# Kernel tuning notes

Hardware: AMD Instinct MI355X
Metric: run time of the kernel (lower is better)

The kernel has to match this reference:

```python
import jax, jax.numpy as jnp
import numpy as np

B, S, D, H, L, FF = 32, 512, 256, 8, 2, 512
E = 64  # embed_dim_per_feature
VOCABS = [20, 50, 100]
NCLS = 36
MAX_CONN, THR = 10, 0.6


def _ln(x, g, b, eps=1e-5):
    m = x.mean(-1, keepdims=True)
    v = ((x - m) ** 2).mean(-1, keepdims=True)
    return g * (x - m) / jnp.sqrt(v + eps) + b


def _build_adj(cat, cnt):
    # self loops + chain links + banded similarity links (create_mutation_graph_optimized)
    Bb, _, Ss = cat.shape
    adj = jnp.broadcast_to(jnp.eye(Ss, dtype=jnp.float32), (Bb, Ss, Ss))
    for d in range(1, MAX_CONN):
        if d >= Ss:
            break
        cat_sim = (cat[:, :, :-d] == cat[:, :, d:]).astype(jnp.float32).mean(1)
        cnt_sim = jnp.exp(-jnp.abs(cnt[:, :-d] - cnt[:, d:]) / 100.0)
        sim = 0.5 * (cat_sim + cnt_sim)  # [B, S-d]
        base = 1.0 if d == 1 else 0.0  # chain link stays 1 when sim<=thr
        val = jnp.where(sim > THR, sim, base)
        ii = jnp.arange(Ss - d)
        adj = adj.at[:, ii, ii + d].set(val)
        adj = adj.at[:, ii + d, ii].set(val)
    return adj


def setup_inputs():
    key = jax.random.key(0)
    ks = iter(jax.random.split(key, 40))
    def nrm(shape, s=0.02):
        return jax.random.normal(next(ks), shape, jnp.float32) * s
    return {
        "categorical_x": jax.random.randint(next(ks), (B, 3, S), 0, min(VOCABS)),
        "count_x": jax.random.uniform(next(ks), (B, S), jnp.float32) * 100.0,
        "emb0": nrm((VOCABS[0], E)), "emb1": nrm((VOCABS[1], E)), "emb2": nrm((VOCABS[2], E)),
        "cnt_W": nrm((1, E)), "cnt_b": jnp.zeros((E,), jnp.float32),
        "pos_enc": nrm((S, D)),
        "gat_W": nrm((L, D, D)), "gat_a": nrm((L, 2 * D, 1)),
        "qkv_W": nrm((L, 3 * D, D)), "qkv_b": jnp.zeros((L, 3 * D), jnp.float32),
        "outp_W": nrm((L, D, D)), "outp_b": jnp.zeros((L, D), jnp.float32),
        "ff1_W": nrm((L, FF, D)), "ff1_b": jnp.zeros((L, FF), jnp.float32),
        "ff2_W": nrm((L, D, FF)), "ff2_b": jnp.zeros((L, D), jnp.float32),
        "ln_g": jnp.ones((L, 3, D), jnp.float32), "ln_b": jnp.zeros((L, 3, D), jnp.float32),
        "cls1_W": nrm((D // 2, D)), "cls1_b": jnp.zeros((D // 2,), jnp.float32),
        "cls2_W": nrm((NCLS, D // 2)), "cls2_b": jnp.zeros((NCLS,), jnp.float32),
    }


def reference(categorical_x, count_x, emb0, emb1, emb2, cnt_W, cnt_b, pos_enc,
              gat_W, gat_a, qkv_W, qkv_b, outp_W, outp_b,
              ff1_W, ff1_b, ff2_W, ff2_b, ln_g, ln_b,
              cls1_W, cls1_b, cls2_W, cls2_b):
    Ss = categorical_x.shape[2]
    # per-timestep feature embedding + count projection, concat -> d_model
    x = jnp.concatenate([
        emb0[categorical_x[:, 0]], emb1[categorical_x[:, 1]], emb2[categorical_x[:, 2]],
        count_x[..., None] @ cnt_W + cnt_b], -1)
    x = x + pos_enc[:Ss]
    mask = _build_adj(categorical_x, count_x) > 0  # adj used only as mask
    dh = D // H
    for l in range(L):
        # GraphAttentionLayer: e_ij = Wh_i.a1 + Wh_j.a2 (same math as repeat+concat+matmul)
        Wh = x @ gat_W[l]
        e = (Wh @ gat_a[l][:D, 0])[:, :, None] + (Wh @ gat_a[l][D:, 0])[:, None, :]
        att = jax.nn.softmax(jnp.where(mask, e, -9e15), -1)
        g = jax.nn.elu(att @ Wh)
        x = _ln(x + g, ln_g[l, 0], ln_b[l, 0])
        # MultiheadAttention (batch_first, eval)
        qkv = x @ qkv_W[l].T + qkv_b[l]
        q, k, v = jnp.split(qkv, 3, -1)
        q = q.reshape(-1, Ss, H, dh)
        k = k.reshape(-1, Ss, H, dh)
        v = v.reshape(-1, Ss, H, dh)
        sc = jnp.einsum('bihd,bjhd->bhij', q, k) / jnp.sqrt(jnp.float32(dh))
        o = jnp.einsum('bhij,bjhd->bihd', jax.nn.softmax(sc, -1), v).reshape(-1, Ss, D)
        o = o @ outp_W[l].T + outp_b[l]
        x = _ln(x + o, ln_g[l, 1], ln_b[l, 1])
        # FFN
        ff = jax.nn.relu(x @ ff1_W[l].T + ff1_b[l]) @ ff2_W[l].T + ff2_b[l]
        x = _ln(x + ff, ln_g[l, 2], ln_b[l, 2])
    pooled = x.mean(1)
    h = jax.nn.relu(pooled @ cls1_W.T + cls1_b)
    return h @ cls2_W.T + cls2_b
```

## Files before the change

kernel.cpp:

```cpp
#include <hip/hip_runtime.h>
#include <hip/hip_bf16.h>
#include <math.h>

#define Bn 32
#define Sn 512
#define Dn 256
#define Hn 8
#define DHn 32
#define En 64
#define FFn 512
#define Ln 2
#define NCLSn 36
#define BANDR 9
#define NBn 19
#define Mn (Bn * Sn)

typedef __attribute__((ext_vector_type(8))) short s8v;
typedef __attribute__((ext_vector_type(4))) float f4v;
typedef __attribute__((ext_vector_type(4))) unsigned short us4;
typedef unsigned short ushortT;

__device__ __forceinline__ ushortT f2b(float f) {
    unsigned u = __float_as_uint(f);
    unsigned r = (u + 0x7FFFu + ((u >> 16) & 1u)) >> 16;
    return (ushortT)r;
}

#define GLDS16(g, l)                                                            \
    __builtin_amdgcn_global_load_lds(                                           \
        (const __attribute__((address_space(1))) void*)(g),                     \
        (__attribute__((address_space(3))) void*)(l), 16, 0, 0)

__global__ void k_f2b(const float* __restrict__ in, ushortT* __restrict__ out, int n) {
    int i = (blockIdx.x * blockDim.x + threadIdx.x) * 4;
    if (i >= n) return;
    float4 v = *(const float4*)(in + i);
    out[i + 0] = f2b(v.x); out[i + 1] = f2b(v.y);
    out[i + 2] = f2b(v.z); out[i + 3] = f2b(v.w);
}

__global__ void k_f2bT(const float* __restrict__ in, ushortT* __restrict__ out) {
    int i = blockIdx.x * 256 + threadIdx.x;
    int l = i >> 16, rem = i & 65535;
    int k = rem >> 8, n = rem & 255;
    out[(l << 16) + n * 256 + k] = f2b(in[i]);
}

__global__ void k_embed(const int* __restrict__ cat, const float* __restrict__ cnt,
                        const float* __restrict__ e0, const float* __restrict__ e1,
                        const float* __restrict__ e2,
                        const float* __restrict__ cW, const float* __restrict__ cb,
                        const float* __restrict__ pos, float* __restrict__ x,
                        ushortT* __restrict__ xb) {
    int bs = blockIdx.x;
    int d = threadIdx.x;
    int b = bs >> 9, s = bs & 511;
    float v;
    if (d < 64)       v = e0[cat[(b * 3 + 0) * Sn + s] * En + d];
    else if (d < 128) v = e1[cat[(b * 3 + 1) * Sn + s] * En + (d - 64)];
    else if (d < 192) v = e2[cat[(b * 3 + 2) * Sn + s] * En + (d - 128)];
    else              v = cnt[b * Sn + s] * cW[d - 192] + cb[d - 192];
    float y = v + pos[s * Dn + d];
    x[(size_t)bs * Dn + d] = y;
    xb[(size_t)bs * Dn + d] = f2b(y);
}

__global__ void k_mask(const int* __restrict__ cat, const float* __restrict__ cnt,
                       unsigned char* __restrict__ mask) {
    int idx = blockIdx.x * blockDim.x + threadIdx.x;
    if (idx >= Bn * Sn * NBn) return;
    int off = idx % NBn;
    int bs = idx / NBn;
    int b = bs >> 9, i = bs & 511;
    int j = i + off - BANDR;
    unsigned char m = 0;
    if (j >= 0 && j < Sn) {
        int dd = off - BANDR;
        int ad = dd < 0 ? -dd : dd;
        if (ad <= 1) {
            m = 1;
        } else {
            int c = 0;
            for (int f = 0; f < 3; f++)
                c += (cat[(b * 3 + f) * Sn + i] == cat[(b * 3 + f) * Sn + j]);
            float cat_sim = (float)c / 3.0f;
            float cnt_sim = expf(-fabsf(cnt[b * Sn + i] - cnt[b * Sn + j]) / 100.0f);
            float sim = 0.5f * (cat_sim + cnt_sim);
            m = (sim > 0.6f) ? 1 : 0;
        }
    }
    mask[idx] = m;
}

template <int ACT>
__global__ __launch_bounds__(256) void k_gemm_mfma(const ushortT* __restrict__ A,
                                                   const ushortT* __restrict__ Bt,
                                                   const float* __restrict__ bias,
                                                   ushortT* __restrict__ Cout,
                                                   int M, int N, int K) {
    __shared__ ushortT As[2][128 * 32];
    __shared__ ushortT Bs[2][128 * 32];
    int tid = threadIdx.x;
    int w = tid >> 6, lane = tid & 63;
    int g = lane >> 4, lr = lane & 15;
    int m0 = blockIdx.y * 128, n0 = blockIdx.x * 128;
    int wr = w >> 1, wc = w & 1;
    int NT = K >> 5;
    f4v acc[4][4];
#pragma unroll
    for (int m = 0; m < 4; m++)
#pragma unroll
        for (int n = 0; n < 4; n++) acc[m][n] = (f4v){0.f, 0.f, 0.f, 0.f};

    auto stage = [&](int t, int buf) {
        int k0 = t << 5;
#pragma unroll
        for (int r = 0; r < 2; r++) {
            int e = (tid + r * 256) * 8;
            int row = e >> 5, kk = e & 31;
            GLDS16(A + (size_t)(m0 + row) * K + k0 + kk, &As[buf][e]);
            GLDS16(Bt + (size_t)(n0 + row) * K + k0 + kk, &Bs[buf][e]);
        }
    };

    stage(0, 0);
    __syncthreads();
    for (int t = 0; t < NT; t++) {
        int cur = t & 1;
        if (t + 1 < NT) stage(t + 1, cur ^ 1);
        s8v af[4], bf[4];
#pragma unroll
        for (int m = 0; m < 4; m++)
            af[m] = *(const s8v*)(&As[cur][(wr * 64 + m * 16 + lr) * 32 + g * 8]);
#pragma unroll
        for (int n = 0; n < 4; n++)
            bf[n] = *(const s8v*)(&Bs[cur][(wc * 64 + n * 16 + lr) * 32 + g * 8]);
#pragma unroll
        for (int m = 0; m < 4; m++)
#pragma unroll
            for (int n = 0; n < 4; n++)
                acc[m][n] = __builtin_amdgcn_mfma_f32_16x16x32_bf16(af[m], bf[n], acc[m][n], 0, 0, 0);
        __syncthreads();
    }
#pragma unroll
    for (int m = 0; m < 4; m++) {
#pragma unroll
        for (int n = 0; n < 4; n++) {
            int col = n0 + wc * 64 + n * 16 + lr;
            float bv = bias ? bias[col] : 0.0f;
#pragma unroll
            for (int r = 0; r < 4; r++) {
                int row = m0 + wr * 64 + m * 16 + g * 4 + r;
                float v = acc[m][n][r] + bv;
                if (ACT == 1) v = fmaxf(v, 0.0f);
                Cout[(size_t)row * N + col] = f2b(v);
            }
        }
    }
}

template <int MODE>
__global__ __launch_bounds__(512) void k_gemm_row(const ushortT* __restrict__ A,
                                                  const ushortT* __restrict__ Bt,
                                                  const float* __restrict__ bias,
                                                  const float* __restrict__ ga,
                                                  float* __restrict__ a1h, float* __restrict__ a2h,
                                                  float* __restrict__ Whout,
                                                  const float* __restrict__ lg,
                                                  const float* __restrict__ lb,
                                                  float* __restrict__ x, ushortT* __restrict__ xb,
                                                  int K) {
    __shared__ ushortT As[2][64 * 32];
    __shared__ ushortT Bs[2][256 * 32];
    __shared__ float red1[64][4], red2[64][4];
    int tid = threadIdx.x;
    int w = tid >> 6, lane = tid & 63;
    int g = lane >> 4, lr = lane & 15;
    int wr = w >> 2, wc = w & 3;
    int m0 = blockIdx.x * 64;
    int NT = K >> 5;
    f4v acc[2][4];
#pragma unroll
    for (int m = 0; m < 2; m++)
#pragma unroll
        for (int n = 0; n < 4; n++) acc[m][n] = (f4v){0.f, 0.f, 0.f, 0.f};

    auto stage = [&](int t, int buf) {
        int k0 = t << 5;
        if (tid < 256) {
            int e = tid * 8;
            int row = e >> 5, kk = e & 31;
            GLDS16(A + (size_t)(m0 + row) * K + k0 + kk, &As[buf][e]);
        }
#pragma unroll
        for (int r = 0; r < 2; r++) {
            int e = (tid + r * 512) * 8;
            int row = e >> 5, kk = e & 31;
            GLDS16(Bt + (size_t)row * K + k0 + kk, &Bs[buf][e]);
        }
    };

    stage(0, 0);
    __syncthreads();
    for (int t = 0; t < NT; t++) {
        int cur = t & 1;
        if (t + 1 < NT) stage(t + 1, cur ^ 1);
        s8v af[2], bf[4];
#pragma unroll
        for (int m = 0; m < 2; m++)
            af[m] = *(const s8v*)(&As[cur][(wr * 32 + m * 16 + lr) * 32 + g * 8]);
#pragma unroll
        for (int n = 0; n < 4; n++)
            bf[n] = *(const s8v*)(&Bs[cur][(wc * 64 + n * 16 + lr) * 32 + g * 8]);
#pragma unroll
        for (int m = 0; m < 2; m++)
#pragma unroll
            for (int n = 0; n < 4; n++)
                acc[m][n] = __builtin_amdgcn_mfma_f32_16x16x32_bf16(af[m], bf[n], acc[m][n], 0, 0, 0);
        __syncthreads();
    }

    int cn[4];
#pragma unroll
    for (int n = 0; n < 4; n++) cn[n] = wc * 64 + n * 16 + lr;

    if constexpr (MODE == 0) {
        float a1v[4], a2v[4];
#pragma unroll
        for (int n = 0; n < 4; n++) { a1v[n] = ga[cn[n]]; a2v[n] = ga[Dn + cn[n]]; }
#pragma unroll
        for (int m = 0; m < 2; m++)
#pragma unroll
            for (int r = 0; r < 4; r++) {
                int rowl = wr * 32 + m * 16 + g * 4 + r;
                float p1 = 0.f, p2 = 0.f;
#pragma unroll
                for (int n = 0; n < 4; n++) {
                    float v = acc[m][n][r];
                    Whout[(size_t)(m0 + rowl) * Dn + cn[n]] = v;
                    p1 += v * a1v[n];
                    p2 += v * a2v[n];
                }
                p1 += __shfl_xor(p1, 1); p2 += __shfl_xor(p2, 1);
                p1 += __shfl_xor(p1, 2); p2 += __shfl_xor(p2, 2);
                p1 += __shfl_xor(p1, 4); p2 += __shfl_xor(p2, 4);
                p1 += __shfl_xor(p1, 8); p2 += __shfl_xor(p2, 8);
                if (lr == 0) { red1[rowl][wc] = p1; red2[rowl][wc] = p2; }
            }
        __syncthreads();
        if (tid < 64) {
            float t1 = red1[tid][0] + red1[tid][1] + red1[tid][2] + red1[tid][3];
            float t2 = red2[tid][0] + red2[tid][1] + red2[tid][2] + red2[tid][3];
            a1h[m0 + tid] = t1;
            a2h[m0 + tid] = t2;
        }
    } else {
        float bv[4], lgv[4], lbv[4];
#pragma unroll
        for (int n = 0; n < 4; n++) { bv[n] = bias[cn[n]]; lgv[n] = lg[cn[n]]; lbv[n] = lb[cn[n]]; }
#pragma unroll
        for (int m = 0; m < 2; m++)
#pragma unroll
            for (int r = 0; r < 4; r++) {
                int rowl = wr * 32 + m * 16 + g * 4 + r;
                float s1 = 0.f, s2 = 0.f;
#pragma unroll
                for (int n = 0; n < 4; n++) {
                    float y = acc[m][n][r] + bv[n] + x[(size_t)(m0 + rowl) * Dn + cn[n]];
                    acc[m][n][r] = y;
                    s1 += y;
                    s2 += y * y;
                }
                s1 += __shfl_xor(s1, 1); s2 += __shfl_xor(s2, 1);
                s1 += __shfl_xor(s1, 2); s2 += __shfl_xor(s2, 2);
                s1 += __shfl_xor(s1, 4); s2 += __shfl_xor(s2, 4);
                s1 += __shfl_xor(s1, 8); s2 += __shfl_xor(s2, 8);
                if (lr == 0) { red1[rowl][wc] = s1; red2[rowl][wc] = s2; }
            }
        __syncthreads();
#pragma unroll
        for (int m = 0; m < 2; m++)
#pragma unroll
            for (int r = 0; r < 4; r++) {
                int rowl = wr * 32 + m * 16 + g * 4 + r;
                float S1 = red1[rowl][0] + red1[rowl][1] + red1[rowl][2] + red1[rowl][3];
                float S2 = red2[rowl][0] + red2[rowl][1] + red2[rowl][2] + red2[rowl][3];
                float mean = S1 * (1.0f / Dn);
                float var = S2 * (1.0f / Dn) - mean * mean;
                float rs = rsqrtf(var + 1e-5f);
#pragma unroll
                for (int n = 0; n < 4; n++) {
                    float o = lgv[n] * (acc[m][n][r] - mean) * rs + lbv[n];
                    size_t idx = (size_t)(m0 + rowl) * Dn + cn[n];
                    x[idx] = o;
                    xb[idx] = f2b(o);
                }
            }
    }
}

__global__ __launch_bounds__(256) void k_gat_attn_ln(const float* __restrict__ Wh,
                                                     const float* __restrict__ a1h,
                                                     const float* __restrict__ a2h,
                                                     const unsigned char* __restrict__ mask,
                                                     const float* __restrict__ lg,
                                                     const float* __restrict__ lb,
                                                     float* __restrict__ x,
                                                     ushortT* __restrict__ xb) {
    int w = threadIdx.x >> 6, l = threadIdx.x & 63;
    int bs = blockIdx.x * 4 + w;
    int b = bs >> 9, i = bs & 511;
    float e = -1e30f;
    int j = i + l - BANDR;
    if (l < NBn && j >= 0 && j < Sn && mask[bs * NBn + l])
        e = a1h[bs] + a2h[(b << 9) + j];
    float mx = e;
#pragma unroll
    for (int o = 32; o; o >>= 1) mx = fmaxf(mx, __shfl_xor(mx, o));
    float p = (e > -1e29f) ? __expf(e - mx) : 0.0f;
    float sum = p;
#pragma unroll
    for (int o = 32; o; o >>= 1) sum += __shfl_xor(sum, o);
    p *= (1.0f / sum);
    int c4 = l * 4;
    const float* whb = Wh + (size_t)(b << 9) * Dn + c4;
    float gx = 0.f, gy = 0.f, gz = 0.f, gw = 0.f;
#pragma unroll
    for (int o = 0; o < NBn; o++) {
        float wo = __shfl(p, o);
        int jo = i + o - BANDR;
        jo = jo < 0 ? 0 : (jo > Sn - 1 ? Sn - 1 : jo);
        float4 v = *(const float4*)(whb + (size_t)jo * Dn);
        gx += wo * v.x; gy += wo * v.y; gz += wo * v.z; gw += wo * v.w;
    }
    gx = gx > 0.f ? gx : expm1f(gx);
    gy = gy > 0.f ? gy : expm1f(gy);
    gz = gz > 0.f ? gz : expm1f(gz);
    gw = gw > 0.f ? gw : expm1f(gw);
    float4 xv = *(const float4*)(x + (size_t)bs * Dn + c4);
    float y0 = xv.x + gx, y1 = xv.y + gy, y2 = xv.z + gz, y3 = xv.w + gw;
    float s1 = y0 + y1 + y2 + y3;
    float s2 = y0 * y0 + y1 * y1 + y2 * y2 + y3 * y3;
#pragma unroll
    for (int o = 32; o; o >>= 1) {
        s1 += __shfl_xor(s1, o);
        s2 += __shfl_xor(s2, o);
    }
    float mean = s1 * (1.0f / Dn);
    float var = s2 * (1.0f / Dn) - mean * mean;
    float r = rsqrtf(var + 1e-5f);
    float4 lgv = *(const float4*)(lg + c4);
    float4 lbv = *(const float4*)(lb + c4);
    float o0 = lgv.x * (y0 - mean) * r + lbv.x;
    float o1 = lgv.y * (y1 - mean) * r + lbv.y;
    float o2 = lgv.z * (y2 - mean) * r + lbv.z;
    float o3 = lgv.w * (y3 - mean) * r + lbv.w;
    *(float4*)(x + (size_t)bs * Dn + c4) = make_float4(o0, o1, o2, o3);
    us4 ob = {f2b(o0), f2b(o1), f2b(o2), f2b(o3)};
    *(us4*)(xb + (size_t)bs * Dn + c4) = ob;
}

__global__ __launch_bounds__(256) void k_attn_mfma(const ushortT* __restrict__ qkv,
                                                   ushortT* __restrict__ ob) {
    __shared__ ushortT Ks[2][64 * 32];
    __shared__ ushortT Vt[2][32 * 64];
    __shared__ ushortT Ps[4][16 * 72];
    int tid = threadIdx.x;
    int w = tid >> 6, lane = tid & 63;
    int g = lane >> 4, lr = lane & 15;
    int blk = blockIdx.x;
    int qh = blk & 1, h = (blk >> 1) & 7, b = blk >> 4;
    const ushortT* base = qkv + (size_t)b * Sn * 768;
    const ushortT* kbase = base + 256 + h * 32;
    const ushortT* vbase = base + 512 + h * 32;

    int krow2 = tid >> 3;
    int kc = (tid & 7) ^ (krow2 & 7);
    int kkv = krow2 * 2 + (kc >> 2);
    int kdd = (kc & 3) * 8;
    int vd0 = w * 8;

    int q0 = qh * 256 + w * 64;
    s8v qf[4];
#pragma unroll
    for (int m = 0; m < 4; m++)
        qf[m] = *(const s8v*)(base + (size_t)(q0 + m * 16 + lr) * 768 + h * 32 + g * 8);

    f4v o[4][2];
    float rl[4][4];
#pragma unroll
    for (int m = 0; m < 4; m++) {
        o[m][0] = (f4v){0.f, 0.f, 0.f, 0.f};
        o[m][1] = (f4v){0.f, 0.f, 0.f, 0.f};
#pragma unroll
        for (int r = 0; r < 4; r++) rl[m][r] = 0.f;
    }
    const float scale = 0.17677669529663687f;

    {
        GLDS16(kbase + (size_t)kkv * 768 + kdd, &Ks[0][tid * 8]);
        us4 v0 = *(const us4*)(vbase + (size_t)lane * 768 + vd0);
        us4 v1 = *(const us4*)(vbase + (size_t)lane * 768 + vd0 + 4);
#pragma unroll
        for (int jj = 0; jj < 4; jj++) {
            int d = vd0 + jj;
            Vt[0][d * 64 + (lane ^ ((d & 7) << 3))] = v0[jj];
            int d2 = d + 4;
            Vt[0][d2 * 64 + (lane ^ ((d2 & 7) << 3))] = v1[jj];
        }
    }
    __syncthreads();

    for (int kt = 0; kt < 8; kt++) {
        int cur = kt & 1, nxt = cur ^ 1;
        us4 v0, v1;
        if (kt < 7) {
            GLDS16(kbase + (size_t)((kt + 1) * 64 + kkv) * 768 + kdd, &Ks[nxt][tid * 8]);
            v0 = *(const us4*)(vbase + (size_t)((kt + 1) * 64 + lane) * 768 + vd0);
            v1 = *(const us4*)(vbase + (size_t)((kt + 1) * 64 + lane) * 768 + vd0 + 4);
        }
        s8v kf[4];
#pragma unroll
        for (int n = 0; n < 4; n++) {
            int row2 = n * 8 + (lr >> 1);
            int cc = (((lr & 1) << 2) + g) ^ (row2 & 7);
            kf[n] = *(const s8v*)(&Ks[cur][row2 * 64 + cc * 8]);
        }
        s8v vf[2][2];
#pragma unroll
        for (int cd = 0; cd < 2; cd++)
#pragma unroll
            for (int c2 = 0; c2 < 2; c2++) {
                int d = cd * 16 + lr;
                vf[cd][c2] = *(const s8v*)(&Vt[cur][d * 64 + ((c2 * 32 + g * 8) ^ ((d & 7) << 3))]);
            }
#pragma unroll
        for (int m = 0; m < 4; m++) {
            f4v s[4];
#pragma unroll
            for (int n = 0; n < 4; n++) {
                f4v z = (f4v){0.f, 0.f, 0.f, 0.f};
                s[n] = __builtin_amdgcn_mfma_f32_16x16x32_bf16(qf[m], kf[n], z, 0, 0, 0);
            }
#pragma unroll
            for (int r = 0; r < 4; r++) {
                float p0 = __expf(fminf(s[0][r] * scale, 60.f));
                float p1 = __expf(fminf(s[1][r] * scale, 60.f));
                float p2 = __expf(fminf(s[2][r] * scale, 60.f));
                float p3 = __expf(fminf(s[3][r] * scale, 60.f));
                rl[m][r] += (p0 + p1) + (p2 + p3);
                int rr = g * 4 + r;
                Ps[w][rr * 72 + lr]      = f2b(p0);
                Ps[w][rr * 72 + 16 + lr] = f2b(p1);
                Ps[w][rr * 72 + 32 + lr] = f2b(p2);
                Ps[w][rr * 72 + 48 + lr] = f2b(p3);
            }
            s8v pf0 = *(const s8v*)(&Ps[w][lr * 72 + g * 8]);
            s8v pf1 = *(const s8v*)(&Ps[w][lr * 72 + 32 + g * 8]);
            o[m][0] = __builtin_amdgcn_mfma_f32_16x16x32_bf16(pf0, vf[0][0], o[m][0], 0, 0, 0);
            o[m][0] = __builtin_amdgcn_mfma_f32_16x16x32_bf16(pf1, vf[0][1], o[m][0], 0, 0, 0);
            o[m][1] = __builtin_amdgcn_mfma_f32_16x16x32_bf16(pf0, vf[1][0], o[m][1], 0, 0, 0);
            o[m][1] = __builtin_amdgcn_mfma_f32_16x16x32_bf16(pf1, vf[1][1], o[m][1], 0, 0, 0);
        }
        if (kt < 7) {
#pragma unroll
            for (int jj = 0; jj < 4; jj++) {
                int d = vd0 + jj;
                Vt[nxt][d * 64 + (lane ^ ((d & 7) << 3))] = v0[jj];
                int d2 = d + 4;
                Vt[nxt][d2 * 64 + (lane ^ ((d2 & 7) << 3))] = v1[jj];
            }
        }
        __syncthreads();
    }
#pragma unroll
    for (int m = 0; m < 4; m++) {
#pragma unroll
        for (int r = 0; r < 4; r++) {
            float t = rl[m][r];
            t += __shfl_xor(t, 1);
            t += __shfl_xor(t, 2);
            t += __shfl_xor(t, 4);
            t += __shfl_xor(t, 8);
            float inv = 1.0f / t;
            int qr = q0 + m * 16 + g * 4 + r;
            size_t obase = ((size_t)(b * Sn + qr)) * Dn + h * 32;
            ob[obase + lr] = f2b(o[m][0][r] * inv);
            ob[obase + 16 + lr] = f2b(o[m][1][r] * inv);
        }
    }
}

__global__ void k_pool(const float* __restrict__ x, float* __restrict__ part) {
    int b = blockIdx.x, sc = blockIdx.y;
    int t = threadIdx.x;
    float s = 0.f;
    for (int s0 = 0; s0 < 64; s0++)
        s += x[((size_t)(b << 9) + sc * 64 + s0) * Dn + t];
    part[(b * 8 + sc) * Dn + t] = s;
}

__global__ void k_cls(const float* __restrict__ part, const float* __restrict__ w1,
                      const float* __restrict__ b1, const float* __restrict__ w2,
                      const float* __restrict__ b2, float* __restrict__ out) {
    int b = blockIdx.x;
    int t = threadIdx.x;
    __shared__ float pooled[Dn];
    __shared__ float hbuf[128];
    float s = 0.f;
#pragma unroll
    for (int k = 0; k < 8; k++) s += part[(b * 8 + k) * Dn + t];
    pooled[t] = s * (1.0f / Sn);
    __syncthreads();
    if (t < 128) {
        float a = b1[t];
        for (int k = 0; k < Dn; k++) a += pooled[k] * w1[t * Dn + k];
        hbuf[t] = fmaxf(a, 0.0f);
    }
    __syncthreads();
    if (t < NCLSn) {
        float a2 = b2[t];
        for (int k = 0; k < 128; k++) a2 += hbuf[k] * w2[t * 128 + k];
        out[b * NCLSn + t] = a2;
    }
}

extern "C" void kernel_launch(void* const* d_in, const int* in_sizes, int n_in,
                              void* d_out, int out_size, void* d_ws, size_t ws_size,
                              hipStream_t stream) {
    const int* cat = (const int*)d_in[0];
    const float* cnt = (const float*)d_in[1];
    const float* emb0 = (const float*)d_in[2];
    const float* emb1 = (const float*)d_in[3];
    const float* emb2 = (const float*)d_in[4];
    const float* cnt_W = (const float*)d_in[5];
    const float* cnt_b = (const float*)d_in[6];
    const float* pos_enc = (const float*)d_in[7];
    const float* gat_W = (const float*)d_in[8];
    const float* gat_a = (const float*)d_in[9];
    const float* qkv_W = (const float*)d_in[10];
    const float* qkv_b = (const float*)d_in[11];
    const float* outp_W = (const float*)d_in[12];
    const float* outp_b = (const float*)d_in[13];
    const float* ff1_W = (const float*)d_in[14];
    const float* ff1_b = (const float*)d_in[15];
    const float* ff2_W = (const float*)d_in[16];
    const float* ff2_b = (const float*)d_in[17];
    const float* ln_g = (const float*)d_in[18];
    const float* ln_b = (const float*)d_in[19];
    const float* cls1_W = (const float*)d_in[20];
    const float* cls1_b = (const float*)d_in[21];
    const float* cls2_W = (const float*)d_in[22];
    const float* cls2_b = (const float*)d_in[23];
    float* out = (float*)d_out;

    char* wp = (char*)d_ws;
    float* x = (float*)wp;        wp += (size_t)Mn * Dn * 4;
    float* tmpf = (float*)wp;     wp += (size_t)Mn * Dn * 4;
    ushortT* xb = (ushortT*)wp;   wp += (size_t)Mn * Dn * 2;
    ushortT* qkvb = (ushortT*)wp; wp += (size_t)Mn * 3 * Dn * 2;
    ushortT* ffb = qkvb;
    ushortT* obb = (ushortT*)wp;  wp += (size_t)Mn * Dn * 2;
    float* a1h = (float*)wp;      wp += (size_t)Mn * 4;
    float* a2h = (float*)wp;      wp += (size_t)Mn * 4;
    float* part = (float*)wp;     wp += (size_t)Bn * 8 * Dn * 4;
    unsigned char* mask = (unsigned char*)wp; wp += (size_t)Mn * NBn;
    ushortT* gatWb = (ushortT*)wp;  wp += (size_t)Ln * Dn * Dn * 2;
    ushortT* qkvWb = (ushortT*)wp;  wp += (size_t)Ln * 3 * Dn * Dn * 2;
    ushortT* outpWb = (ushortT*)wp; wp += (size_t)Ln * Dn * Dn * 2;
    ushortT* ff1Wb = (ushortT*)wp;  wp += (size_t)Ln * FFn * Dn * 2;
    ushortT* ff2Wb = (ushortT*)wp;  wp += (size_t)Ln * Dn * FFn * 2;

    k_f2bT<<<Ln * 65536 / 256, 256, 0, stream>>>(gat_W, gatWb);
    k_f2b<<<(Ln * 3 * Dn * Dn / 4 + 255) / 256, 256, 0, stream>>>(qkv_W, qkvWb, Ln * 3 * Dn * Dn);
    k_f2b<<<(Ln * Dn * Dn / 4 + 255) / 256, 256, 0, stream>>>(outp_W, outpWb, Ln * Dn * Dn);
    k_f2b<<<(Ln * FFn * Dn / 4 + 255) / 256, 256, 0, stream>>>(ff1_W, ff1Wb, Ln * FFn * Dn);
    k_f2b<<<(Ln * Dn * FFn / 4 + 255) / 256, 256, 0, stream>>>(ff2_W, ff2Wb, Ln * Dn * FFn);

    k_embed<<<Mn, Dn, 0, stream>>>(cat, cnt, emb0, emb1, emb2, cnt_W, cnt_b, pos_enc, x, xb);
    k_mask<<<(Bn * Sn * NBn + 255) / 256, 256, 0, stream>>>(cat, cnt, mask);

    for (int l = 0; l < Ln; l++) {
        k_gemm_row<0><<<Mn / 64, 512, 0, stream>>>(
            xb, gatWb + (size_t)l * Dn * Dn, nullptr,
            gat_a + (size_t)l * 2 * Dn, a1h, a2h, tmpf,
            nullptr, nullptr, nullptr, nullptr, Dn);
        k_gat_attn_ln<<<Mn / 4, 256, 0, stream>>>(tmpf, a1h, a2h, mask,
                                                  ln_g + (l * 3 + 0) * Dn, ln_b + (l * 3 + 0) * Dn, x, xb);
        k_gemm_mfma<0><<<dim3(3 * Dn / 128, Mn / 128), 256, 0, stream>>>(
            xb, qkvWb + (size_t)l * 3 * Dn * Dn, qkv_b + l * 3 * Dn, qkvb, Mn, 3 * Dn, Dn);
        k_attn_mfma<<<Bn * Hn * 2, 256, 0, stream>>>(qkvb, obb);
        k_gemm_row<1><<<Mn / 64, 512, 0, stream>>>(
            obb, outpWb + (size_t)l * Dn * Dn, outp_b + l * Dn,
            nullptr, nullptr, nullptr, nullptr,
            ln_g + (l * 3 + 1) * Dn, ln_b + (l * 3 + 1) * Dn, x, xb, Dn);
        k_gemm_mfma<1><<<dim3(FFn / 128, Mn / 128), 256, 0, stream>>>(
            xb, ff1Wb + (size_t)l * FFn * Dn, ff1_b + l * FFn, ffb, Mn, FFn, Dn);
        k_gemm_row<1><<<Mn / 64, 512, 0, stream>>>(
            ffb, ff2Wb + (size_t)l * Dn * FFn, ff2_b + l * Dn,
            nullptr, nullptr, nullptr, nullptr,
            ln_g + (l * 3 + 2) * Dn, ln_b + (l * 3 + 2) * Dn, x, xb, FFn);
    }

    k_pool<<<dim3(Bn, 8), 256, 0, stream>>>(x, part);
    k_cls<<<Bn, Dn, 0, stream>>>(part, cls1_W, cls1_b, cls2_W, cls2_b, out);
}
```

Measured before the change: 317.6 us.

## Merge prep kernels, remap workgroups across XCDs, split attention queries finer

```diff
diff --git a/kernel.cpp b/kernel.cpp
--- a/kernel.cpp
+++ b/kernel.cpp
@@ -31,65 +31,75 @@
         (const __attribute__((address_space(1))) void*)(g),                     \
         (__attribute__((address_space(3))) void*)(l), 16, 0, 0)
 
-__global__ void k_f2b(const float* __restrict__ in, ushortT* __restrict__ out, int n) {
-    int i = (blockIdx.x * blockDim.x + threadIdx.x) * 4;
-    if (i >= n) return;
-    float4 v = *(const float4*)(in + i);
-    out[i + 0] = f2b(v.x); out[i + 1] = f2b(v.y);
-    out[i + 2] = f2b(v.z); out[i + 3] = f2b(v.w);
-}
-
-__global__ void k_f2bT(const float* __restrict__ in, ushortT* __restrict__ out) {
-    int i = blockIdx.x * 256 + threadIdx.x;
-    int l = i >> 16, rem = i & 65535;
-    int k = rem >> 8, n = rem & 255;
-    out[(l << 16) + n * 256 + k] = f2b(in[i]);
-}
-
-__global__ void k_embed(const int* __restrict__ cat, const float* __restrict__ cnt,
-                        const float* __restrict__ e0, const float* __restrict__ e1,
-                        const float* __restrict__ e2,
-                        const float* __restrict__ cW, const float* __restrict__ cb,
-                        const float* __restrict__ pos, float* __restrict__ x,
-                        ushortT* __restrict__ xb) {
-    int bs = blockIdx.x;
-    int d = threadIdx.x;
-    int b = bs >> 9, s = bs & 511;
-    float v;
-    if (d < 64)       v = e0[cat[(b * 3 + 0) * Sn + s] * En + d];
-    else if (d < 128) v = e1[cat[(b * 3 + 1) * Sn + s] * En + (d - 64)];
-    else if (d < 192) v = e2[cat[(b * 3 + 2) * Sn + s] * En + (d - 128)];
-    else              v = cnt[b * Sn + s] * cW[d - 192] + cb[d - 192];
-    float y = v + pos[s * Dn + d];
-    x[(size_t)bs * Dn + d] = y;
-    xb[(size_t)bs * Dn + d] = f2b(y);
-}
-
-__global__ void k_mask(const int* __restrict__ cat, const float* __restrict__ cnt,
-                       unsigned char* __restrict__ mask) {
-    int idx = blockIdx.x * blockDim.x + threadIdx.x;
-    if (idx >= Bn * Sn * NBn) return;
-    int off = idx % NBn;
-    int bs = idx / NBn;
-    int b = bs >> 9, i = bs & 511;
-    int j = i + off - BANDR;
-    unsigned char m = 0;
-    if (j >= 0 && j < Sn) {
-        int dd = off - BANDR;
-        int ad = dd < 0 ? -dd : dd;
-        if (ad <= 1) {
-            m = 1;
-        } else {
-            int c = 0;
-            for (int f = 0; f < 3; f++)
-                c += (cat[(b * 3 + f) * Sn + i] == cat[(b * 3 + f) * Sn + j]);
-            float cat_sim = (float)c / 3.0f;
-            float cnt_sim = expf(-fabsf(cnt[b * Sn + i] - cnt[b * Sn + j]) / 100.0f);
-            float sim = 0.5f * (cat_sim + cnt_sim);
-            m = (sim > 0.6f) ? 1 : 0;
-        }
-    }
-    mask[idx] = m;
+__global__ void k_f2b_all(const float* __restrict__ qkvW, const float* __restrict__ outpW,
+                          const float* __restrict__ ff1W, const float* __restrict__ ff2W,
+                          const float* __restrict__ gatW,
+                          ushortT* __restrict__ qkvWb, ushortT* __restrict__ outpWb,
+                          ushortT* __restrict__ ff1Wb, ushortT* __restrict__ ff2Wb,
+                          ushortT* __restrict__ gatWb) {
+    int bid = blockIdx.x;
+    if (bid < 1024) {
+        int i4 = bid * 256 + threadIdx.x;
+        const float* src; ushortT* dst; int off;
+        if (i4 < 98304)       { src = qkvW;  dst = qkvWb;  off = 0; }
+        else if (i4 < 131072) { src = outpW; dst = outpWb; off = 98304; }
+        else if (i4 < 196608) { src = ff1W;  dst = ff1Wb;  off = 131072; }
+        else                  { src = ff2W;  dst = ff2Wb;  off = 196608; }
+        int j = (i4 - off) * 4;
+        float4 v = *(const float4*)(src + j);
+        us4 o = {f2b(v.x), f2b(v.y), f2b(v.z), f2b(v.w)};
+        *(us4*)(dst + j) = o;
+    } else {
+        int i = (bid - 1024) * 256 + threadIdx.x;
+        int l = i >> 16, rem = i & 65535;
+        int k = rem >> 8, n = rem & 255;
+        gatWb[(l << 16) + n * 256 + k] = f2b(gatW[i]);
+    }
+}
+
+__global__ void k_embed_mask(const int* __restrict__ cat, const float* __restrict__ cnt,
+                             const float* __restrict__ e0, const float* __restrict__ e1,
+                             const float* __restrict__ e2,
+                             const float* __restrict__ cW, const float* __restrict__ cb,
+                             const float* __restrict__ pos, float* __restrict__ x,
+                             ushortT* __restrict__ xb, unsigned char* __restrict__ maskp) {
+    if (blockIdx.x < Mn) {
+        int bs = blockIdx.x;
+        int d = threadIdx.x;
+        int b = bs >> 9, s = bs & 511;
+        float v;
+        if (d < 64)       v = e0[cat[(b * 3 + 0) * Sn + s] * En + d];
+        else if (d < 128) v = e1[cat[(b * 3 + 1) * Sn + s] * En + (d - 64)];
+        else if (d < 192) v = e2[cat[(b * 3 + 2) * Sn + s] * En + (d - 128)];
+        else              v = cnt[b * Sn + s] * cW[d - 192] + cb[d - 192];
+        float y = v + pos[s * Dn + d];
+        x[(size_t)bs * Dn + d] = y;
+        xb[(size_t)bs * Dn + d] = f2b(y);
+    } else {
+        int idx = (blockIdx.x - Mn) * 256 + threadIdx.x;
+        if (idx >= Bn * Sn * NBn) return;
+        int off = idx % NBn;
+        int bs = idx / NBn;
+        int b = bs >> 9, i = bs & 511;
+        int j = i + off - BANDR;
+        unsigned char m = 0;
+        if (j >= 0 && j < Sn) {
+            int dd = off - BANDR;
+            int ad = dd < 0 ? -dd : dd;
+            if (ad <= 1) {
+                m = 1;
+            } else {
+                int c = 0;
+                for (int f = 0; f < 3; f++)
+                    c += (cat[(b * 3 + f) * Sn + i] == cat[(b * 3 + f) * Sn + j]);
+                float cat_sim = (float)c / 3.0f;
+                float cnt_sim = expf(-fabsf(cnt[b * Sn + i] - cnt[b * Sn + j]) / 100.0f);
+                float sim = 0.5f * (cat_sim + cnt_sim);
+                m = (sim > 0.6f) ? 1 : 0;
+            }
+        }
+        maskp[idx] = m;
+    }
 }
 
 template <int ACT>
@@ -103,7 +113,10 @@
     int tid = threadIdx.x;
     int w = tid >> 6, lane = tid & 63;
     int g = lane >> 4, lr = lane & 15;
-    int m0 = blockIdx.y * 128, n0 = blockIdx.x * 128;
+    int o_ = blockIdx.y * gridDim.x + blockIdx.x;
+    int nwg = gridDim.x * gridDim.y;
+    int wid = (o_ & 7) * (nwg >> 3) + (o_ >> 3);
+    int m0 = (wid / gridDim.x) * 128, n0 = (wid % gridDim.x) * 128;
     int wr = w >> 1, wc = w & 1;
     int NT = K >> 5;
     f4v acc[4][4];
@@ -177,7 +190,9 @@
     int w = tid >> 6, lane = tid & 63;
     int g = lane >> 4, lr = lane & 15;
     int wr = w >> 2, wc = w & 3;
-    int m0 = blockIdx.x * 64;
+    int o_ = blockIdx.x;
+    int wid = (o_ & 7) * (gridDim.x >> 3) + (o_ >> 3);
+    int m0 = wid * 64;
     int NT = K >> 5;
     f4v acc[2][4];
 #pragma unroll
@@ -364,12 +379,13 @@
                                                    ushortT* __restrict__ ob) {
     __shared__ ushortT Ks[2][64 * 32];
     __shared__ ushortT Vt[2][32 * 64];
-    __shared__ ushortT Ps[4][16 * 72];
+    __shared__ ushortT Ps[4][32 * 72];
     int tid = threadIdx.x;
     int w = tid >> 6, lane = tid & 63;
     int g = lane >> 4, lr = lane & 15;
-    int blk = blockIdx.x;
-    int qh = blk & 1, h = (blk >> 1) & 7, b = blk >> 4;
+    int o_ = blockIdx.x;
+    int blk = (o_ & 7) * (gridDim.x >> 3) + (o_ >> 3);
+    int qq = blk & 3, h = (blk >> 2) & 7, b = blk >> 5;
     const ushortT* base = qkv + (size_t)b * Sn * 768;
     const ushortT* kbase = base + 256 + h * 32;
     const ushortT* vbase = base + 512 + h * 32;
@@ -380,22 +396,22 @@
     int kdd = (kc & 3) * 8;
     int vd0 = w * 8;
 
-    int q0 = qh * 256 + w * 64;
-    s8v qf[4];
-#pragma unroll
-    for (int m = 0; m < 4; m++)
+    int q0 = qq * 128 + w * 32;
+    s8v qf[2];
+#pragma unroll
+    for (int m = 0; m < 2; m++)
         qf[m] = *(const s8v*)(base + (size_t)(q0 + m * 16 + lr) * 768 + h * 32 + g * 8);
 
-    f4v o[4][2];
-    float rl[4][4];
-#pragma unroll
-    for (int m = 0; m < 4; m++) {
+    f4v o[2][2];
+    float rl[2][4];
+#pragma unroll
+    for (int m = 0; m < 2; m++) {
         o[m][0] = (f4v){0.f, 0.f, 0.f, 0.f};
         o[m][1] = (f4v){0.f, 0.f, 0.f, 0.f};
 #pragma unroll
         for (int r = 0; r < 4; r++) rl[m][r] = 0.f;
     }
-    const float scale = 0.17677669529663687f;
+    const float scale2 = 0.25506973f;
 
     {
         GLDS16(kbase + (size_t)kkv * 768 + kdd, &Ks[0][tid * 8]);
@@ -434,29 +450,33 @@
                 int d = cd * 16 + lr;
                 vf[cd][c2] = *(const s8v*)(&Vt[cur][d * 64 + ((c2 * 32 + g * 8) ^ ((d & 7) << 3))]);
             }
-#pragma unroll
-        for (int m = 0; m < 4; m++) {
-            f4v s[4];
+        f4v s[2][4];
+#pragma unroll
+        for (int m = 0; m < 2; m++)
 #pragma unroll
             for (int n = 0; n < 4; n++) {
                 f4v z = (f4v){0.f, 0.f, 0.f, 0.f};
-                s[n] = __builtin_amdgcn_mfma_f32_16x16x32_bf16(qf[m], kf[n], z, 0, 0, 0);
-            }
+                s[m][n] = __builtin_amdgcn_mfma_f32_16x16x32_bf16(qf[m], kf[n], z, 0, 0, 0);
+            }
+#pragma unroll
+        for (int m = 0; m < 2; m++)
 #pragma unroll
             for (int r = 0; r < 4; r++) {
-                float p0 = __expf(fminf(s[0][r] * scale, 60.f));
-                float p1 = __expf(fminf(s[1][r] * scale, 60.f));
-                float p2 = __expf(fminf(s[2][r] * scale, 60.f));
-                float p3 = __expf(fminf(s[3][r] * scale, 60.f));
+                float p0 = exp2f(fminf(s[m][0][r] * scale2, 86.f));
+                float p1 = exp2f(fminf(s[m][1][r] * scale2, 86.f));
+                float p2 = exp2f(fminf(s[m][2][r] * scale2, 86.f));
+                float p3 = exp2f(fminf(s[m][3][r] * scale2, 86.f));
                 rl[m][r] += (p0 + p1) + (p2 + p3);
-                int rr = g * 4 + r;
+                int rr = m * 16 + g * 4 + r;
                 Ps[w][rr * 72 + lr]      = f2b(p0);
                 Ps[w][rr * 72 + 16 + lr] = f2b(p1);
                 Ps[w][rr * 72 + 32 + lr] = f2b(p2);
                 Ps[w][rr * 72 + 48 + lr] = f2b(p3);
             }
-            s8v pf0 = *(const s8v*)(&Ps[w][lr * 72 + g * 8]);
-            s8v pf1 = *(const s8v*)(&Ps[w][lr * 72 + 32 + g * 8]);
+#pragma unroll
+        for (int m = 0; m < 2; m++) {
+            s8v pf0 = *(const s8v*)(&Ps[w][(m * 16 + lr) * 72 + g * 8]);
+            s8v pf1 = *(const s8v*)(&Ps[w][(m * 16 + lr) * 72 + 32 + g * 8]);
             o[m][0] = __builtin_amdgcn_mfma_f32_16x16x32_bf16(pf0, vf[0][0], o[m][0], 0, 0, 0);
             o[m][0] = __builtin_amdgcn_mfma_f32_16x16x32_bf16(pf1, vf[0][1], o[m][0], 0, 0, 0);
             o[m][1] = __builtin_amdgcn_mfma_f32_16x16x32_bf16(pf0, vf[1][0], o[m][1], 0, 0, 0);
@@ -474,7 +494,7 @@
         __syncthreads();
     }
 #pragma unroll
-    for (int m = 0; m < 4; m++) {
+    for (int m = 0; m < 2; m++) {
 #pragma unroll
         for (int r = 0; r < 4; r++) {
             float t = rl[m][r];
@@ -491,25 +511,16 @@
     }
 }
 
-__global__ void k_pool(const float* __restrict__ x, float* __restrict__ part) {
-    int b = blockIdx.x, sc = blockIdx.y;
-    int t = threadIdx.x;
-    float s = 0.f;
-    for (int s0 = 0; s0 < 64; s0++)
-        s += x[((size_t)(b << 9) + sc * 64 + s0) * Dn + t];
-    part[(b * 8 + sc) * Dn + t] = s;
-}
-
-__global__ void k_cls(const float* __restrict__ part, const float* __restrict__ w1,
-                      const float* __restrict__ b1, const float* __restrict__ w2,
-                      const float* __restrict__ b2, float* __restrict__ out) {
+__global__ void k_pool_cls(const float* __restrict__ x, const float* __restrict__ w1,
+                           const float* __restrict__ b1, const float* __restrict__ w2,
+                           const float* __restrict__ b2, float* __restrict__ out) {
     int b = blockIdx.x;
     int t = threadIdx.x;
     __shared__ float pooled[Dn];
     __shared__ float hbuf[128];
     float s = 0.f;
-#pragma unroll
-    for (int k = 0; k < 8; k++) s += part[(b * 8 + k) * Dn + t];
+    const float* xp = x + (size_t)(b << 9) * Dn + t;
+    for (int sx = 0; sx < Sn; sx++) s += xp[(size_t)sx * Dn];
     pooled[t] = s * (1.0f / Sn);
     __syncthreads();
     if (t < 128) {
@@ -563,7 +574,6 @@
     ushortT* obb = (ushortT*)wp;  wp += (size_t)Mn * Dn * 2;
     float* a1h = (float*)wp;      wp += (size_t)Mn * 4;
     float* a2h = (float*)wp;      wp += (size_t)Mn * 4;
-    float* part = (float*)wp;     wp += (size_t)Bn * 8 * Dn * 4;
     unsigned char* mask = (unsigned char*)wp; wp += (size_t)Mn * NBn;
     ushortT* gatWb = (ushortT*)wp;  wp += (size_t)Ln * Dn * Dn * 2;
     ushortT* qkvWb = (ushortT*)wp;  wp += (size_t)Ln * 3 * Dn * Dn * 2;
@@ -571,14 +581,10 @@
     ushortT* ff1Wb = (ushortT*)wp;  wp += (size_t)Ln * FFn * Dn * 2;
     ushortT* ff2Wb = (ushortT*)wp;  wp += (size_t)Ln * Dn * FFn * 2;
 
-    k_f2bT<<<Ln * 65536 / 256, 256, 0, stream>>>(gat_W, gatWb);
-    k_f2b<<<(Ln * 3 * Dn * Dn / 4 + 255) / 256, 256, 0, stream>>>(qkv_W, qkvWb, Ln * 3 * Dn * Dn);
-    k_f2b<<<(Ln * Dn * Dn / 4 + 255) / 256, 256, 0, stream>>>(outp_W, outpWb, Ln * Dn * Dn);
-    k_f2b<<<(Ln * FFn * Dn / 4 + 255) / 256, 256, 0, stream>>>(ff1_W, ff1Wb, Ln * FFn * Dn);
-    k_f2b<<<(Ln * Dn * FFn / 4 + 255) / 256, 256, 0, stream>>>(ff2_W, ff2Wb, Ln * Dn * FFn);
-
-    k_embed<<<Mn, Dn, 0, stream>>>(cat, cnt, emb0, emb1, emb2, cnt_W, cnt_b, pos_enc, x, xb);
-    k_mask<<<(Bn * Sn * NBn + 255) / 256, 256, 0, stream>>>(cat, cnt, mask);
+    k_f2b_all<<<1536, 256, 0, stream>>>(qkv_W, outp_W, ff1_W, ff2_W, gat_W,
+                                        qkvWb, outpWb, ff1Wb, ff2Wb, gatWb);
+    k_embed_mask<<<Mn + 1216, 256, 0, stream>>>(cat, cnt, emb0, emb1, emb2, cnt_W, cnt_b,
+                                                pos_enc, x, xb, mask);
 
     for (int l = 0; l < Ln; l++) {
         k_gemm_row<0><<<Mn / 64, 512, 0, stream>>>(
@@ -589,7 +595,7 @@
                                                   ln_g + (l * 3 + 0) * Dn, ln_b + (l * 3 + 0) * Dn, x, xb);
         k_gemm_mfma<0><<<dim3(3 * Dn / 128, Mn / 128), 256, 0, stream>>>(
             xb, qkvWb + (size_t)l * 3 * Dn * Dn, qkv_b + l * 3 * Dn, qkvb, Mn, 3 * Dn, Dn);
-        k_attn_mfma<<<Bn * Hn * 2, 256, 0, stream>>>(qkvb, obb);
+        k_attn_mfma<<<Bn * Hn * 4, 256, 0, stream>>>(qkvb, obb);
         k_gemm_row<1><<<Mn / 64, 512, 0, stream>>>(
             obb, outpWb + (size_t)l * Dn * Dn, outp_b + l * Dn,
             nullptr, nullptr, nullptr, nullptr,
@@ -602,6 +608,5 @@
             ln_g + (l * 3 + 2) * Dn, ln_b + (l * 3 + 2) * Dn, x, xb, FFn);
     }
 
-    k_pool<<<dim3(Bn, 8), 256, 0, stream>>>(x, part);
-    k_cls<<<Bn, Dn, 0, stream>>>(part, cls1_W, cls1_b, cls2_W, cls2_b, out);
-}
+    k_pool_cls<<<Bn, 256, 0, stream>>>(x, cls1_W, cls1_b, cls2_W, cls2_b, out);
+}
```

New measurement: 321.5 us. No clear change (+1.2%).
